# Performance work log

Measured on AMD Instinct MI355X. Metric: run time of the kernel, lower is better.

The kernel has to match this reference:

```python
import jax, jax.numpy as jnp
import numpy as np

D_MODEL, D_K, D_V, H, GRID = 512, 64, 64, 8, 196
B = 4


def setup_inputs() -> dict:
    key = jax.random.key(0)
    ks = jax.random.split(key, 12)
    s = 0.02
    return {
        "queries": jax.random.normal(ks[0], (B, GRID, D_MODEL), jnp.float32),
        "keys": jax.random.normal(ks[1], (B, GRID, D_MODEL), jnp.float32),
        "values": jax.random.normal(ks[2], (B, GRID, D_MODEL), jnp.float32),
        "Wq": jax.random.normal(ks[3], (H * D_K, D_MODEL), jnp.float32) * s,
        "bq": jnp.zeros((H * D_K,), jnp.float32),
        "Wk": jax.random.normal(ks[4], (H * D_K, D_MODEL), jnp.float32) * s,
        "bk": jnp.zeros((H * D_K,), jnp.float32),
        "Wv": jax.random.normal(ks[5], (H * D_V, D_MODEL), jnp.float32) * s,
        "bv": jnp.zeros((H * D_V,), jnp.float32),
        "Wo": jax.random.normal(ks[6], (D_MODEL, H * D_V), jnp.float32) * s,
        "bo": jnp.zeros((D_MODEL,), jnp.float32),
        "scale": jnp.ones((1, H, GRID, GRID), jnp.float32) / np.sqrt(D_K).astype(np.float32),
    }


def reference(queries, keys, values, Wq, bq, Wk, bk, Wv, bv, Wo, bo, scale):
    b, nq, _ = queries.shape
    nk = values.shape[1]
    # linear projections (torch nn.Linear: x @ W.T + b)
    q_sig = queries @ Wq.T + bq          # (b, nq, h*dk)
    k_p = keys @ Wk.T + bk               # (b, nk, h*dk)
    v_p = values @ Wv.T + bv             # (b, nk, h*dv)
    # elementwise q*k interaction (b, nq, nk, h*dk)
    att_e = q_sig[:, :, None, :] * k_p[:, None, :, :]
    # sigmoid-gated values
    v_g = jax.nn.sigmoid(att_e) * v_p[:, None, :, :]
    v = v_g.reshape(b, nq, nk, H, D_K).transpose(0, 3, 1, 2, 4)      # (b,h,nq,nk,dk)
    att = att_e.reshape(b, nq, nk, H, D_K).transpose(0, 3, 1, 2, 4)  # (b,h,nq,nk,dk)
    att = att.sum(-1) * scale            # (b,h,nq,nk)
    p = jax.nn.softmax(att, axis=-1)     # dropout is identity in eval mode
    # (att.unsqueeze(-2) @ v).squeeze(-2)
    image = jnp.einsum("bhqk,bhqkd->bhqd", p, v)
    image = image.transpose(0, 2, 1, 3).reshape(b, nq, H * D_V)
    out = image @ Wo.T + bo              # (b, nq, d_model)
    out = jax.nn.sigmoid(q_sig * out) * out
    return out
```

## Files before the change

### kernel.cpp

```cpp
#include <hip/hip_runtime.h>
#include <hip/hip_bf16.h>
#include <math.h>

#define NQ 196
#define BATCH 4
#define HD 512
#define NH 8
#define DK 64
#define MROWS 784
#define MPAD 832

typedef __attribute__((ext_vector_type(8))) short short8;
typedef __attribute__((ext_vector_type(4))) short short4v;
typedef __attribute__((ext_vector_type(4))) float float4v;

__device__ __forceinline__ float b2f(short s) {
  return __uint_as_float(((unsigned)(unsigned short)s) << 16);
}
__device__ __forceinline__ short f2b(float x) {
  return __builtin_bit_cast(short, __float2bfloat16(x));
}
__device__ __forceinline__ float fexp2(float x) {
  float r; asm("v_exp_f32 %0, %1" : "=v"(r) : "v"(x)); return r;
}
__device__ __forceinline__ float frcp(float x) {
  float r; asm("v_rcp_f32 %0, %1" : "=v"(r) : "v"(x)); return r;
}
__device__ __forceinline__ void cvt4(float4 v, short4v& hi, short4v& lo) {
  float x[4] = {v.x, v.y, v.z, v.w};
  #pragma unroll
  for (int i = 0; i < 4; ++i) {
    hi[i] = f2b(x[i]);
    lo[i] = f2b(x[i] - b2f(hi[i]));
  }
}
__device__ __forceinline__ void gload_lds16(const void* g, void* l) {
  __builtin_amdgcn_global_load_lds(
      (const __attribute__((address_space(1))) unsigned int*)g,
      (__attribute__((address_space(3))) unsigned int*)l, 16, 0, 0);
}

struct WSplitArgs { const float* src[4]; short* hi[4]; short* lo[4]; };

__global__ __launch_bounds__(256)
void wsplit_kernel(WSplitArgs a) {
  const int seg = blockIdx.x >> 7;
  const size_t off = (size_t)(blockIdx.x & 127) * 2048 + (size_t)threadIdx.x * 8;
  const float* src = a.src[seg] + off;
  float4 v0 = *(const float4*)(src);
  float4 v1 = *(const float4*)(src + 4);
  short4v h0, l0, h1, l1;
  cvt4(v0, h0, l0); cvt4(v1, h1, l1);
  short8 vh = {h0[0],h0[1],h0[2],h0[3],h1[0],h1[1],h1[2],h1[3]};
  short8 vl = {l0[0],l0[1],l0[2],l0[3],l1[0],l1[1],l1[2],l1[3]};
  *(short8*)(a.hi[seg] + off) = vh;
  *(short8*)(a.lo[seg] + off) = vl;
}

struct GemmArgs {
  const float* X[3]; const short* Wh[3]; const short* Wl[3]; const float* bias[3];
  float* Cf[3]; short* Ch[3]; short* Cl[3]; const float* gate[3];
};

__global__ __launch_bounds__(512)
void mgemm(GemmArgs p, int M, int N, int K) {
  const int z = blockIdx.z;
  const float* __restrict__ X  = p.X[z];
  const short* __restrict__ Wh = p.Wh[z];
  const short* __restrict__ Wl = p.Wl[z];

  __shared__ short smem[24576];
  short* const A_ = smem;
  short* const B_ = smem + 8192;
  float* const redC = (float*)smem;

  const int t = threadIdx.x;
  const int g = t >> 8;
  const int tt = t & 255;
  const int ln = t & 63, lm = ln & 15, quad = ln >> 4;
  const int w = (t >> 6) & 3;
  const int m0 = blockIdx.x * 32, n0 = blockIdx.y * 64;
  const int kb = g << 8;

  const int aRow = tt >> 3, aK = (tt & 7) << 2;
  const int ar = min(m0 + aRow, M - 1);
  const float* Ap = X + (size_t)ar * K + kb + aK;
  const int aIdx = aRow * 32 + aK;
  const int bRow = tt >> 2, bK = (tt & 3) << 3;
  const short* Bph = Wh + (size_t)(n0 + bRow) * K + kb + bK;
  const short* Bpl = Wl + (size_t)(n0 + bRow) * K + kb + bK;

  const int wm = (w & 1) << 4, wn = (w >> 1) << 5;
  float4v acc[2] = {{0.f,0.f,0.f,0.f},{0.f,0.f,0.f,0.f}};

  const int T = 8;
  float4 ra = *(const float4*)Ap;
  gload_lds16(Bph, &B_[((g << 1) + 0) * 4096 + 0 * 2048 + tt * 8]);
  gload_lds16(Bpl, &B_[((g << 1) + 0) * 4096 + 1 * 2048 + tt * 8]);
  {
    short4v ahi, alo; cvt4(ra, ahi, alo);
    *(short4v*)&A_[((g << 1) + 0) * 2048 + 0 * 1024 + aIdx] = ahi;
    *(short4v*)&A_[((g << 1) + 0) * 2048 + 1 * 1024 + aIdx] = alo;
  }

  for (int kt = 0; kt < T; ++kt) {
    const int buf = kt & 1;
    __syncthreads();
    if (kt + 1 < T) {
      ra = *(const float4*)(Ap + (size_t)(kt + 1) * 32);
      const int nb = buf ^ 1;
      gload_lds16(Bph + (size_t)(kt + 1) * 32, &B_[((g << 1) + nb) * 4096 + 0 * 2048 + tt * 8]);
      gload_lds16(Bpl + (size_t)(kt + 1) * 32, &B_[((g << 1) + nb) * 4096 + 1 * 2048 + tt * 8]);
    }
    const short* Ab = &A_[((g << 1) + buf) * 2048];
    const short* Bb = &B_[((g << 1) + buf) * 4096];
    short8 fah = *(const short8*)&Ab[0 * 1024 + (wm + lm) * 32 + (quad << 3)];
    short8 fal = *(const short8*)&Ab[1 * 1024 + (wm + lm) * 32 + (quad << 3)];
    #pragma unroll
    for (int ni = 0; ni < 2; ++ni) {
      short8 fbh = *(const short8*)&Bb[0 * 2048 + (wn + (ni << 4) + lm) * 32 + (quad << 3)];
      short8 fbl = *(const short8*)&Bb[1 * 2048 + (wn + (ni << 4) + lm) * 32 + (quad << 3)];
      acc[ni] = __builtin_amdgcn_mfma_f32_16x16x32_bf16(fah, fbh, acc[ni], 0,0,0);
      acc[ni] = __builtin_amdgcn_mfma_f32_16x16x32_bf16(fah, fbl, acc[ni], 0,0,0);
      acc[ni] = __builtin_amdgcn_mfma_f32_16x16x32_bf16(fal, fbh, acc[ni], 0,0,0);
    }
    if (kt + 1 < T) {
      const int nb = buf ^ 1;
      short4v ahi, alo; cvt4(ra, ahi, alo);
      *(short4v*)&A_[((g << 1) + nb) * 2048 + 0 * 1024 + aIdx] = ahi;
      *(short4v*)&A_[((g << 1) + nb) * 2048 + 1 * 1024 + aIdx] = alo;
    }
  }

  __syncthreads();
  if (g == 1) {
    #pragma unroll
    for (int ni = 0; ni < 2; ++ni)
      *(float4v*)&redC[tt * 8 + ni * 4] = acc[ni];
  }
  __syncthreads();
  if (g == 0) {
    const float* bias = p.bias[z];
    const float* gate = p.gate[z];
    float* Cf = p.Cf[z]; short* Ch = p.Ch[z]; short* Cl = p.Cl[z];
    #pragma unroll
    for (int ni = 0; ni < 2; ++ni) {
      const int n = n0 + wn + (ni << 4) + lm;
      const float bv = bias[n];
      #pragma unroll
      for (int r = 0; r < 4; ++r) {
        const int m = m0 + wm + (quad << 2) + r;
        if (m < M) {
          float c = acc[ni][r] + redC[tt * 8 + ni * 4 + r] + bv;
          if (gate) {
            const float qg = gate[(size_t)m * N + n];
            c = __fdividef(c, 1.f + __expf(-qg * c));
          }
          if (Cf) Cf[(size_t)m * N + n] = c;
          if (Ch) {
            const short hi = f2b(c);
            Ch[(size_t)m * N + n] = hi;
            Cl[(size_t)m * N + n] = f2b(c - b2f(hi));
          }
        }
      }
    }
  }
}

__global__ __launch_bounds__(256)
void attn_fused(const short* __restrict__ qsh, const short* __restrict__ qsl,
                const short* __restrict__ ksh, const short* __restrict__ ksl,
                const float* __restrict__ qsg, const float* __restrict__ kpg,
                const float* __restrict__ vpg, const float* __restrict__ scg,
                float* __restrict__ img) {
  const int q0 = blockIdx.x * 16;
  const int h  = blockIdx.y;
  const int b  = blockIdx.z;
  const int t  = threadIdx.x;
  const int w = t >> 6, ln = t & 63;
  const int lm = ln & 15, quad = ln >> 4;
  const float L2E = 1.4426950408889634f;

  __shared__ float S[16][210];
  __shared__ float R[4][16][64];

  const size_t abase = ((size_t)(b * NQ) + q0 + lm) * HD + h * DK + (quad << 3);
  short8 ah0 = *(const short8*)(qsh + abase);
  short8 ah1 = *(const short8*)(qsh + abase + 32);
  short8 al0 = *(const short8*)(qsl + abase);
  short8 al1 = *(const short8*)(qsl + abase + 32);

  for (int nt = w; nt < 13; nt += 4) {
    const size_t bbase = ((size_t)(b * NQ) + nt * 16 + lm) * HD + h * DK + (quad << 3);
    short8 bh0 = *(const short8*)(ksh + bbase);
    short8 bh1 = *(const short8*)(ksh + bbase + 32);
    short8 bl0 = *(const short8*)(ksl + bbase);
    short8 bl1 = *(const short8*)(ksl + bbase + 32);
    float4v acc = {0.f, 0.f, 0.f, 0.f};
    acc = __builtin_amdgcn_mfma_f32_16x16x32_bf16(ah0, bh0, acc, 0,0,0);
    acc = __builtin_amdgcn_mfma_f32_16x16x32_bf16(ah1, bh1, acc, 0,0,0);
    acc = __builtin_amdgcn_mfma_f32_16x16x32_bf16(ah0, bl0, acc, 0,0,0);
    acc = __builtin_amdgcn_mfma_f32_16x16x32_bf16(ah1, bl1, acc, 0,0,0);
    acc = __builtin_amdgcn_mfma_f32_16x16x32_bf16(al0, bh0, acc, 0,0,0);
    acc = __builtin_amdgcn_mfma_f32_16x16x32_bf16(al1, bh1, acc, 0,0,0);
    #pragma unroll
    for (int r = 0; r < 4; ++r)
      S[(quad << 2) + r][nt * 16 + lm] = acc[r];
  }
  __syncthreads();

  for (int i = 0; i < 4; ++i) {
    const int rr = (w << 2) + i;
    const int q = q0 + rr;
    const bool qok = q < NQ;
    const float* srow = scg + ((size_t)h * NQ + (qok ? q : 0)) * NQ;
    float att[4];
    #pragma unroll
    for (int j = 0; j < 4; ++j) {
      const int c = ln + (j << 6);
      att[j] = -1e30f;
      if (c < NQ) att[j] = S[rr][c] * srow[c] * L2E;
    }
    float m = fmaxf(fmaxf(att[0], att[1]), fmaxf(att[2], att[3]));
    #pragma unroll
    for (int off = 32; off; off >>= 1) m = fmaxf(m, __shfl_xor(m, off, 64));
    float e[4], s = 0.f;
    #pragma unroll
    for (int j = 0; j < 4; ++j) { e[j] = fexp2(att[j] - m); s += e[j]; }
    #pragma unroll
    for (int off = 32; off; off >>= 1) s += __shfl_xor(s, off, 64);
    const float rinv = __fdividef(1.f, s);
    #pragma unroll
    for (int j = 0; j < 4; ++j) {
      const int c = ln + (j << 6);
      if (c < NQ) S[rr][c] = e[j] * rinv;
    }
  }
  __syncthreads();

  const int d = ln;
  const int kg = w;
  const float LOG2E = 1.4426950408889634f;

  float nqs[16];
  #pragma unroll
  for (int qi = 0; qi < 16; ++qi) {
    const int row = min(b * NQ + q0 + qi, MROWS - 1);
    nqs[qi] = -qsg[(size_t)row * HD + h * DK + d] * LOG2E;
  }
  const float* kp = kpg + ((size_t)(b * NQ)) * HD + h * DK + d;
  const float* vp = vpg + ((size_t)(b * NQ)) * HD + h * DK + d;

  float acc[16];
  #pragma unroll
  for (int qi = 0; qi < 16; ++qi) acc[qi] = 0.f;

  for (int k = kg * 49; k < kg * 49 + 49; ++k) {
    const float kv = kp[(size_t)k * HD];
    const float vv = vp[(size_t)k * HD];
    #pragma unroll
    for (int qi = 0; qi < 16; ++qi) {
      const float e = fexp2(nqs[qi] * kv);
      const float g = vv * frcp(1.f + e);
      acc[qi] += S[qi][k] * g;
    }
  }
  #pragma unroll
  for (int qi = 0; qi < 16; ++qi) R[kg][qi][d] = acc[qi];
  __syncthreads();

  #pragma unroll
  for (int j = 0; j < 4; ++j) {
    const int idx = t + (j << 8);
    const int qi = idx >> 6, dd = idx & 63;
    const int q = q0 + qi;
    if (q < NQ) {
      const float s = R[0][qi][dd] + R[1][qi][dd] + R[2][qi][dd] + R[3][qi][dd];
      img[((size_t)(b * NQ) + q) * HD + h * DK + dd] = s;
    }
  }
}

extern "C" void kernel_launch(void* const* d_in, const int* in_sizes, int n_in,
                              void* d_out, int out_size, void* d_ws, size_t ws_size,
                              hipStream_t stream) {
  const float* queries = (const float*)d_in[0];
  const float* keys    = (const float*)d_in[1];
  const float* values  = (const float*)d_in[2];
  const float* Wq = (const float*)d_in[3];
  const float* bq = (const float*)d_in[4];
  const float* Wk = (const float*)d_in[5];
  const float* bk = (const float*)d_in[6];
  const float* Wv = (const float*)d_in[7];
  const float* bv = (const float*)d_in[8];
  const float* Wo = (const float*)d_in[9];
  const float* bo = (const float*)d_in[10];
  const float* scale = (const float*)d_in[11];

  char* base = (char*)d_ws;
  const size_t FB = sizeof(float);
  const size_t NELF  = (size_t)MROWS * HD;
  const size_t NELPS = (size_t)MPAD * HD;
  const size_t WEL   = (size_t)HD * HD;

  size_t o = 0;
  float* q_sig = (float*)(base + o); o += NELF * FB;
  float* k_p   = (float*)(base + o); o += NELF * FB;
  float* v_p   = (float*)(base + o); o += NELF * FB;
  float* image = (float*)(base + o); o += NELF * FB;
  short* qsh = (short*)(base + o); o += NELPS * 2;
  short* qsl = (short*)(base + o); o += NELPS * 2;
  short* ksh = (short*)(base + o); o += NELPS * 2;
  short* ksl = (short*)(base + o); o += NELPS * 2;
  short* Wqh = (short*)(base + o); o += WEL * 2;
  short* Wql = (short*)(base + o); o += WEL * 2;
  short* Wkh = (short*)(base + o); o += WEL * 2;
  short* Wkl = (short*)(base + o); o += WEL * 2;
  short* Wvh = (short*)(base + o); o += WEL * 2;
  short* Wvl = (short*)(base + o); o += WEL * 2;
  short* Woh = (short*)(base + o); o += WEL * 2;
  short* Wol = (short*)(base + o); o += WEL * 2;

  WSplitArgs wa;
  wa.src[0] = Wq; wa.hi[0] = Wqh; wa.lo[0] = Wql;
  wa.src[1] = Wk; wa.hi[1] = Wkh; wa.lo[1] = Wkl;
  wa.src[2] = Wv; wa.hi[2] = Wvh; wa.lo[2] = Wvl;
  wa.src[3] = Wo; wa.hi[3] = Woh; wa.lo[3] = Wol;
  wsplit_kernel<<<512, 256, 0, stream>>>(wa);

  GemmArgs gp;
  gp.X[0] = queries; gp.Wh[0] = Wqh; gp.Wl[0] = Wql; gp.bias[0] = bq;
  gp.Cf[0] = q_sig;  gp.Ch[0] = qsh; gp.Cl[0] = qsl; gp.gate[0] = nullptr;
  gp.X[1] = keys;    gp.Wh[1] = Wkh; gp.Wl[1] = Wkl; gp.bias[1] = bk;
  gp.Cf[1] = k_p;    gp.Ch[1] = ksh; gp.Cl[1] = ksl; gp.gate[1] = nullptr;
  gp.X[2] = values;  gp.Wh[2] = Wvh; gp.Wl[2] = Wvl; gp.bias[2] = bv;
  gp.Cf[2] = v_p;    gp.Ch[2] = nullptr; gp.Cl[2] = nullptr; gp.gate[2] = nullptr;
  mgemm<<<dim3(25, HD/64, 3), 512, 0, stream>>>(gp, MROWS, HD, HD);

  attn_fused<<<dim3(13, NH, BATCH), 256, 0, stream>>>(
      qsh, qsl, ksh, ksl, q_sig, k_p, v_p, scale, image);

  GemmArgs go;
  go.X[0] = image; go.Wh[0] = Woh; go.Wl[0] = Wol; go.bias[0] = bo;
  go.Cf[0] = (float*)d_out; go.Ch[0] = nullptr; go.Cl[0] = nullptr; go.gate[0] = q_sig;
  for (int i = 1; i < 3; ++i) {
    go.X[i] = nullptr; go.Wh[i] = nullptr; go.Wl[i] = nullptr; go.bias[i] = nullptr;
    go.Cf[i] = nullptr; go.Ch[i] = nullptr; go.Cl[i] = nullptr; go.gate[i] = nullptr;
  }
  mgemm<<<dim3(25, HD/64, 1), 512, 0, stream>>>(go, MROWS, HD, HD);
}
```

Before: 143.1 us.

## Shrink GEMM M-tile to 16 and double attention block to 512 threads

The projection and output GEMMs now use 16-row M tiles (49 blocks along M instead of 25), each wave computing a single 16x16 output tile. Because 784 divides evenly by 16, the bounds checks are dropped. The attention kernel moves from 256 to 512 threads and splits the sigmoid-gated key loop across 8 wave groups instead of 4, with an 8-way reduction at the end. The aim is more blocks and more waves in flight to hide latency, at the cost of less operand reuse per block and larger reduction buffers.

```diff
diff --git a/kernel.cpp b/kernel.cpp
--- a/kernel.cpp
+++ b/kernel.cpp
@@ -63,15 +63,15 @@
 };
 
 __global__ __launch_bounds__(512)
-void mgemm(GemmArgs p, int M, int N, int K) {
+void mgemm(GemmArgs p, int N, int K) {
   const int z = blockIdx.z;
   const float* __restrict__ X  = p.X[z];
   const short* __restrict__ Wh = p.Wh[z];
   const short* __restrict__ Wl = p.Wl[z];
 
-  __shared__ short smem[24576];
+  __shared__ short smem[20480];
   short* const A_ = smem;
-  short* const B_ = smem + 8192;
+  short* const B_ = smem + 4096;
   float* const redC = (float*)smem;
 
   const int t = threadIdx.x;
@@ -79,96 +79,86 @@
   const int tt = t & 255;
   const int ln = t & 63, lm = ln & 15, quad = ln >> 4;
   const int w = (t >> 6) & 3;
-  const int m0 = blockIdx.x * 32, n0 = blockIdx.y * 64;
+  const int m0 = blockIdx.x * 16, n0 = blockIdx.y * 64;
   const int kb = g << 8;
 
-  const int aRow = tt >> 3, aK = (tt & 7) << 2;
-  const int ar = min(m0 + aRow, M - 1);
-  const float* Ap = X + (size_t)ar * K + kb + aK;
+  const int aRow = (tt & 127) >> 3, aK = (tt & 7) << 2;
+  const bool aload = tt < 128;
+  const float* Ap = X + (size_t)(m0 + aRow) * K + kb + aK;
   const int aIdx = aRow * 32 + aK;
   const int bRow = tt >> 2, bK = (tt & 3) << 3;
   const short* Bph = Wh + (size_t)(n0 + bRow) * K + kb + bK;
   const short* Bpl = Wl + (size_t)(n0 + bRow) * K + kb + bK;
 
-  const int wm = (w & 1) << 4, wn = (w >> 1) << 5;
-  float4v acc[2] = {{0.f,0.f,0.f,0.f},{0.f,0.f,0.f,0.f}};
+  const int wn = w << 4;
+  float4v acc = {0.f, 0.f, 0.f, 0.f};
 
   const int T = 8;
-  float4 ra = *(const float4*)Ap;
-  gload_lds16(Bph, &B_[((g << 1) + 0) * 4096 + 0 * 2048 + tt * 8]);
-  gload_lds16(Bpl, &B_[((g << 1) + 0) * 4096 + 1 * 2048 + tt * 8]);
-  {
+  float4 ra = aload ? *(const float4*)Ap : make_float4(0.f,0.f,0.f,0.f);
+  gload_lds16(Bph, &B_[(((g << 1) + 0) * 2 + 0) * 2048 + tt * 8]);
+  gload_lds16(Bpl, &B_[(((g << 1) + 0) * 2 + 1) * 2048 + tt * 8]);
+  if (aload) {
     short4v ahi, alo; cvt4(ra, ahi, alo);
-    *(short4v*)&A_[((g << 1) + 0) * 2048 + 0 * 1024 + aIdx] = ahi;
-    *(short4v*)&A_[((g << 1) + 0) * 2048 + 1 * 1024 + aIdx] = alo;
+    *(short4v*)&A_[(((g << 1) + 0) * 2 + 0) * 512 + aIdx] = ahi;
+    *(short4v*)&A_[(((g << 1) + 0) * 2 + 1) * 512 + aIdx] = alo;
   }
 
   for (int kt = 0; kt < T; ++kt) {
     const int buf = kt & 1;
     __syncthreads();
     if (kt + 1 < T) {
-      ra = *(const float4*)(Ap + (size_t)(kt + 1) * 32);
+      if (aload) ra = *(const float4*)(Ap + (size_t)(kt + 1) * 32);
       const int nb = buf ^ 1;
-      gload_lds16(Bph + (size_t)(kt + 1) * 32, &B_[((g << 1) + nb) * 4096 + 0 * 2048 + tt * 8]);
-      gload_lds16(Bpl + (size_t)(kt + 1) * 32, &B_[((g << 1) + nb) * 4096 + 1 * 2048 + tt * 8]);
-    }
-    const short* Ab = &A_[((g << 1) + buf) * 2048];
-    const short* Bb = &B_[((g << 1) + buf) * 4096];
-    short8 fah = *(const short8*)&Ab[0 * 1024 + (wm + lm) * 32 + (quad << 3)];
-    short8 fal = *(const short8*)&Ab[1 * 1024 + (wm + lm) * 32 + (quad << 3)];
-    #pragma unroll
-    for (int ni = 0; ni < 2; ++ni) {
-      short8 fbh = *(const short8*)&Bb[0 * 2048 + (wn + (ni << 4) + lm) * 32 + (quad << 3)];
-      short8 fbl = *(const short8*)&Bb[1 * 2048 + (wn + (ni << 4) + lm) * 32 + (quad << 3)];
-      acc[ni] = __builtin_amdgcn_mfma_f32_16x16x32_bf16(fah, fbh, acc[ni], 0,0,0);
-      acc[ni] = __builtin_amdgcn_mfma_f32_16x16x32_bf16(fah, fbl, acc[ni], 0,0,0);
-      acc[ni] = __builtin_amdgcn_mfma_f32_16x16x32_bf16(fal, fbh, acc[ni], 0,0,0);
-    }
+      gload_lds16(Bph + (size_t)(kt + 1) * 32, &B_[(((g << 1) + nb) * 2 + 0) * 2048 + tt * 8]);
+      gload_lds16(Bpl + (size_t)(kt + 1) * 32, &B_[(((g << 1) + nb) * 2 + 1) * 2048 + tt * 8]);
+    }
+    const short* Ab = &A_[((g << 1) + buf) * 2 * 512];
+    const short* Bb = &B_[((g << 1) + buf) * 2 * 2048];
+    short8 fah = *(const short8*)&Ab[0 * 512 + lm * 32 + (quad << 3)];
+    short8 fal = *(const short8*)&Ab[1 * 512 + lm * 32 + (quad << 3)];
+    short8 fbh = *(const short8*)&Bb[0 * 2048 + (wn + lm) * 32 + (quad << 3)];
+    short8 fbl = *(const short8*)&Bb[1 * 2048 + (wn + lm) * 32 + (quad << 3)];
+    acc = __builtin_amdgcn_mfma_f32_16x16x32_bf16(fah, fbh, acc, 0,0,0);
+    acc = __builtin_amdgcn_mfma_f32_16x16x32_bf16(fah, fbl, acc, 0,0,0);
+    acc = __builtin_amdgcn_mfma_f32_16x16x32_bf16(fal, fbh, acc, 0,0,0);
     if (kt + 1 < T) {
       const int nb = buf ^ 1;
-      short4v ahi, alo; cvt4(ra, ahi, alo);
-      *(short4v*)&A_[((g << 1) + nb) * 2048 + 0 * 1024 + aIdx] = ahi;
-      *(short4v*)&A_[((g << 1) + nb) * 2048 + 1 * 1024 + aIdx] = alo;
-    }
-  }
-
-  __syncthreads();
-  if (g == 1) {
-    #pragma unroll
-    for (int ni = 0; ni < 2; ++ni)
-      *(float4v*)&redC[tt * 8 + ni * 4] = acc[ni];
-  }
+      if (aload) {
+        short4v ahi, alo; cvt4(ra, ahi, alo);
+        *(short4v*)&A_[(((g << 1) + nb) * 2 + 0) * 512 + aIdx] = ahi;
+        *(short4v*)&A_[(((g << 1) + nb) * 2 + 1) * 512 + aIdx] = alo;
+      }
+    }
+  }
+
+  __syncthreads();
+  if (g == 1) *(float4v*)&redC[tt * 4] = acc;
   __syncthreads();
   if (g == 0) {
     const float* bias = p.bias[z];
     const float* gate = p.gate[z];
     float* Cf = p.Cf[z]; short* Ch = p.Ch[z]; short* Cl = p.Cl[z];
-    #pragma unroll
-    for (int ni = 0; ni < 2; ++ni) {
-      const int n = n0 + wn + (ni << 4) + lm;
-      const float bv = bias[n];
-      #pragma unroll
-      for (int r = 0; r < 4; ++r) {
-        const int m = m0 + wm + (quad << 2) + r;
-        if (m < M) {
-          float c = acc[ni][r] + redC[tt * 8 + ni * 4 + r] + bv;
-          if (gate) {
-            const float qg = gate[(size_t)m * N + n];
-            c = __fdividef(c, 1.f + __expf(-qg * c));
-          }
-          if (Cf) Cf[(size_t)m * N + n] = c;
-          if (Ch) {
-            const short hi = f2b(c);
-            Ch[(size_t)m * N + n] = hi;
-            Cl[(size_t)m * N + n] = f2b(c - b2f(hi));
-          }
-        }
+    const int n = n0 + wn + lm;
+    const float bv = bias[n];
+    #pragma unroll
+    for (int r = 0; r < 4; ++r) {
+      const int m = m0 + (quad << 2) + r;
+      float c = acc[r] + redC[tt * 4 + r] + bv;
+      if (gate) {
+        const float qg = gate[(size_t)m * N + n];
+        c = __fdividef(c, 1.f + __expf(-qg * c));
       }
-    }
-  }
-}
-
-__global__ __launch_bounds__(256)
+      if (Cf) Cf[(size_t)m * N + n] = c;
+      if (Ch) {
+        const short hi = f2b(c);
+        Ch[(size_t)m * N + n] = hi;
+        Cl[(size_t)m * N + n] = f2b(c - b2f(hi));
+      }
+    }
+  }
+}
+
+__global__ __launch_bounds__(512)
 void attn_fused(const short* __restrict__ qsh, const short* __restrict__ qsl,
                 const short* __restrict__ ksh, const short* __restrict__ ksl,
                 const float* __restrict__ qsg, const float* __restrict__ kpg,
@@ -183,7 +173,7 @@
   const float L2E = 1.4426950408889634f;
 
   __shared__ float S[16][210];
-  __shared__ float R[4][16][64];
+  __shared__ float R[8][16][64];
 
   const size_t abase = ((size_t)(b * NQ) + q0 + lm) * HD + h * DK + (quad << 3);
   short8 ah0 = *(const short8*)(qsh + abase);
@@ -191,7 +181,7 @@
   short8 al0 = *(const short8*)(qsl + abase);
   short8 al1 = *(const short8*)(qsl + abase + 32);
 
-  for (int nt = w; nt < 13; nt += 4) {
+  for (int nt = w; nt < 13; nt += 8) {
     const size_t bbase = ((size_t)(b * NQ) + nt * 16 + lm) * HD + h * DK + (quad << 3);
     short8 bh0 = *(const short8*)(ksh + bbase);
     short8 bh1 = *(const short8*)(ksh + bbase + 32);
@@ -210,8 +200,8 @@
   }
   __syncthreads();
 
-  for (int i = 0; i < 4; ++i) {
-    const int rr = (w << 2) + i;
+  for (int i = 0; i < 2; ++i) {
+    const int rr = (w << 1) + i;
     const int q = q0 + rr;
     const bool qok = q < NQ;
     const float* srow = scg + ((size_t)h * NQ + (qok ? q : 0)) * NQ;
@@ -241,6 +231,8 @@
 
   const int d = ln;
   const int kg = w;
+  const int kbeg = (kg * 49) >> 1;
+  const int kend = ((kg + 1) * 49) >> 1;
   const float LOG2E = 1.4426950408889634f;
 
   float nqs[16];
@@ -256,7 +248,7 @@
   #pragma unroll
   for (int qi = 0; qi < 16; ++qi) acc[qi] = 0.f;
 
-  for (int k = kg * 49; k < kg * 49 + 49; ++k) {
+  for (int k = kbeg; k < kend; ++k) {
     const float kv = kp[(size_t)k * HD];
     const float vv = vp[(size_t)k * HD];
     #pragma unroll
@@ -271,12 +263,14 @@
   __syncthreads();
 
   #pragma unroll
-  for (int j = 0; j < 4; ++j) {
-    const int idx = t + (j << 8);
+  for (int j = 0; j < 2; ++j) {
+    const int idx = t + (j << 9);
     const int qi = idx >> 6, dd = idx & 63;
     const int q = q0 + qi;
     if (q < NQ) {
-      const float s = R[0][qi][dd] + R[1][qi][dd] + R[2][qi][dd] + R[3][qi][dd];
+      float s = 0.f;
+      #pragma unroll
+      for (int kk = 0; kk < 8; ++kk) s += R[kk][qi][dd];
       img[((size_t)(b * NQ) + q) * HD + h * DK + dd] = s;
     }
   }
@@ -336,9 +330,9 @@
   gp.Cf[1] = k_p;    gp.Ch[1] = ksh; gp.Cl[1] = ksl; gp.gate[1] = nullptr;
   gp.X[2] = values;  gp.Wh[2] = Wvh; gp.Wl[2] = Wvl; gp.bias[2] = bv;
   gp.Cf[2] = v_p;    gp.Ch[2] = nullptr; gp.Cl[2] = nullptr; gp.gate[2] = nullptr;
-  mgemm<<<dim3(25, HD/64, 3), 512, 0, stream>>>(gp, MROWS, HD, HD);
-
-  attn_fused<<<dim3(13, NH, BATCH), 256, 0, stream>>>(
+  mgemm<<<dim3(MROWS/16, HD/64, 3), 512, 0, stream>>>(gp, HD, HD);
+
+  attn_fused<<<dim3(13, NH, BATCH), 512, 0, stream>>>(
       qsh, qsl, ksh, ksl, q_sig, k_p, v_p, scale, image);
 
   GemmArgs go;
@@ -348,5 +342,5 @@
     go.X[i] = nullptr; go.Wh[i] = nullptr; go.Wl[i] = nullptr; go.bias[i] = nullptr;
     go.Cf[i] = nullptr; go.Ch[i] = nullptr; go.Cl[i] = nullptr; go.gate[i] = nullptr;
   }
-  mgemm<<<dim3(25, HD/64, 1), 512, 0, stream>>>(go, MROWS, HD, HD);
-}
+  mgemm<<<dim3(MROWS/16, HD/64, 1), 512, 0, stream>>>(go, HD, HD);
+}
```

After: 138.5 us. 1.03x faster.
